# Optimization experiments

Measured on AMD Instinct MI355X. Metric: run time of the kernel, lower is better.

Reference implementation:

```python
import jax, jax.numpy as jnp
import numpy as np

B = 32768
T = 1024  # num_time_bins


def setup_inputs() -> dict:
    key = jax.random.key(0)
    k1, k2, k3, k4 = jax.random.split(key, 4)
    hazard_values = jax.random.uniform(k1, (B, T), dtype=jnp.float32)
    labels_Y = jax.random.uniform(k2, (B,), dtype=jnp.float32) * T
    # nn.Linear(T, T): weight [T, T] (out, in), bias [T]
    lim = 1.0 / np.sqrt(T)
    W = jax.random.uniform(k3, (T, T), minval=-lim, maxval=lim, dtype=jnp.float32)
    b = jax.random.uniform(k4, (T,), minval=-lim, maxval=lim, dtype=jnp.float32)
    return {"hazard_values": hazard_values, "labels_Y": labels_Y, "W": W, "b": b}


def reference(hazard_values, labels_Y, W, b):
    # linear + sigmoid + argmax -> per-row truncation position
    logits = hazard_values @ W.T + b                       # [B, T]
    trunc_pos = jnp.argmax(jax.nn.sigmoid(logits), axis=1, keepdims=True)  # [B, 1] int
    # survival curve
    S = jnp.cumprod(1.0 - hazard_values, axis=1)           # [B, T]
    # vectorized truncation decay: for t >= p, multiply by exp(-(t - p))
    t = jnp.arange(T)[None, :]                             # [1, T]
    decay = jnp.where(t >= trunc_pos,
                      jnp.exp(-(t - trunc_pos).astype(S.dtype)),
                      jnp.ones((), S.dtype))
    S = S * decay
    # MSE between argmax position and labels (original prints; we skip prints)
    p = trunc_pos[:, 0].astype(jnp.float32)
    truncation_loss = jnp.mean((p - labels_Y) ** 2)
    return trunc_pos, S, truncation_loss
```

## Files before the change

kernel.cpp:

```cpp
#include <hip/hip_runtime.h>

#define B_ROWS 32768
#define T_BINS 1024

typedef __attribute__((ext_vector_type(8))) _Float16 half8;
typedef __attribute__((ext_vector_type(4))) float floatx4;

__device__ __forceinline__ unsigned long long pack_max(float v, int col) {
    unsigned x = __float_as_uint(v);
    x = (x & 0x80000000u) ? ~x : (x | 0x80000000u);
    return ((unsigned long long)x << 32) | (unsigned)(~col);
}

__device__ __forceinline__ void async16h(const _Float16* g, _Float16* l) {
    __builtin_amdgcn_global_load_lds(
        (const __attribute__((address_space(1))) unsigned int*)g,
        (__attribute__((address_space(3))) unsigned int*)l,
        16, 0, 0);
}

__global__ __launch_bounds__(256) void tof16_kernel(
    const float* __restrict__ src, _Float16* __restrict__ dst, int n4)
{
    int idx = blockIdx.x * 256 + threadIdx.x;
    if (idx >= n4) return;
    float4 x = ((const float4*)src)[idx];
    union { _Float16 h[4]; ushort4 u; } cv;
    cv.h[0] = (_Float16)x.x;
    cv.h[1] = (_Float16)x.y;
    cv.h[2] = (_Float16)x.z;
    cv.h[3] = (_Float16)x.w;
    ((ushort4*)dst)[idx] = cv.u;
}

__global__ __launch_bounds__(512, 2) void gemm_argmax_f16(
    const float* __restrict__ A, const _Float16* __restrict__ Wh,
    const float* __restrict__ bias, unsigned long long* __restrict__ rec)
{
    __shared__ _Float16 sA[2][256 * 64];
    __shared__ _Float16 sW[2][256 * 64];

    const int tid  = threadIdx.x;
    const int lane = tid & 63;
    const int w    = tid >> 6;
    const int wr   = w >> 1;
    const int wcl  = w & 1;
    const int slab = blockIdx.x >> 2;
    const int cq   = blockIdx.x & 3;

    const int arow = tid >> 1;
    const int part = tid & 1;
    const int x8a  = (arow ^ (arow >> 3)) & 7;
    const float* Abase = A + (size_t)(slab * 256 + arow) * T_BINS;

    const int l3  = lane >> 3;
    const int wsl = lane & 7;

    const int l15 = lane & 15;
    const int hi  = lane >> 4;

    floatx4 acc[4][8];
#pragma unroll
    for (int i = 0; i < 4; ++i)
#pragma unroll
        for (int j = 0; j < 8; ++j) acc[i][j] = (floatx4){0.f, 0.f, 0.f, 0.f};

#pragma unroll
    for (int s = 0; s < 4; ++s) {
        int ps = part * 4 + s;
        int sc = ps ^ x8a;
        float4 f0 = *(const float4*)(Abase + sc * 8);
        float4 f1 = *(const float4*)(Abase + sc * 8 + 4);
        half8 hv;
        hv[0] = (_Float16)f0.x; hv[1] = (_Float16)f0.y; hv[2] = (_Float16)f0.z; hv[3] = (_Float16)f0.w;
        hv[4] = (_Float16)f1.x; hv[5] = (_Float16)f1.y; hv[6] = (_Float16)f1.z; hv[7] = (_Float16)f1.w;
        *(half8*)&sA[0][arow * 64 + ps * 8] = hv;
    }
#pragma unroll
    for (int r = 0; r < 4; ++r) {
        int cl = w * 32 + r * 8 + l3;
        int sk = wsl ^ ((cl ^ (cl >> 3)) & 7);
        async16h(Wh + (size_t)(cq * 256 + cl) * T_BINS + sk * 8,
                 &sW[0][(w * 32 + r * 8) * 64]);
    }
    __syncthreads();

    for (int t = 0; t < 16; ++t) {
        const int cur = t & 1;
        const int nxt = cur ^ 1;
        const int kn  = ((t + 1) & 15) * 64;

        float4 qa0[4], qa1[4];
#pragma unroll
        for (int s = 0; s < 4; ++s) {
            int sc = (part * 4 + s) ^ x8a;
            qa0[s] = *(const float4*)(Abase + kn + sc * 8);
            qa1[s] = *(const float4*)(Abase + kn + sc * 8 + 4);
        }

#pragma unroll
        for (int r = 0; r < 4; ++r) {
            int cl = w * 32 + r * 8 + l3;
            int sk = wsl ^ ((cl ^ (cl >> 3)) & 7);
            async16h(Wh + (size_t)(cq * 256 + cl) * T_BINS + kn + sk * 8,
                     &sW[nxt][(w * 32 + r * 8) * 64]);
        }

#pragma unroll
        for (int g = 0; g < 2; ++g) {
            half8 ah[4];
#pragma unroll
            for (int i = 0; i < 4; ++i) {
                int rl = wr * 64 + i * 16 + l15;
                int xa = (rl ^ (rl >> 3)) & 7;
                ah[i] = *(const half8*)&sA[cur][rl * 64 + (((g * 4 + hi) ^ xa) * 8)];
            }
#pragma unroll
            for (int jb = 0; jb < 2; ++jb) {
                half8 whf[4];
#pragma unroll
                for (int jj = 0; jj < 4; ++jj) {
                    int cl = wcl * 128 + (jb * 4 + jj) * 16 + l15;
                    int xw = (cl ^ (cl >> 3)) & 7;
                    whf[jj] = *(const half8*)&sW[cur][cl * 64 + (((g * 4 + hi) ^ xw) * 8)];
                }
#pragma unroll
                for (int i = 0; i < 4; ++i)
#pragma unroll
                    for (int jj = 0; jj < 4; ++jj)
                        acc[i][jb * 4 + jj] = __builtin_amdgcn_mfma_f32_16x16x32_f16(
                            ah[i], whf[jj], acc[i][jb * 4 + jj], 0, 0, 0);
            }
        }

#pragma unroll
        for (int s = 0; s < 4; ++s) {
            half8 hv;
            hv[0] = (_Float16)qa0[s].x; hv[1] = (_Float16)qa0[s].y;
            hv[2] = (_Float16)qa0[s].z; hv[3] = (_Float16)qa0[s].w;
            hv[4] = (_Float16)qa1[s].x; hv[5] = (_Float16)qa1[s].y;
            hv[6] = (_Float16)qa1[s].z; hv[7] = (_Float16)qa1[s].w;
            *(half8*)&sA[nxt][arow * 64 + (part * 4 + s) * 8] = hv;
        }

        __syncthreads();
    }

    const int colbase = cq * 256 + wcl * 128 + l15;
    float bj[8];
#pragma unroll
    for (int j = 0; j < 8; ++j) bj[j] = bias[colbase + j * 16];

    unsigned long long (*cand)[256] = reinterpret_cast<unsigned long long (*)[256]>(&sA[0][0]);

#pragma unroll
    for (int i = 0; i < 4; ++i)
#pragma unroll
        for (int r = 0; r < 4; ++r) {
            float best = -3.4e38f;
            int   bc   = 0;
#pragma unroll
            for (int j = 0; j < 8; ++j) {
                float v = acc[i][j][r] + bj[j];
                if (v > best) { best = v; bc = colbase + j * 16; }
            }
#pragma unroll
            for (int off = 8; off >= 1; off >>= 1) {
                float ov = __shfl_xor(best, off, 64);
                int   oc = __shfl_xor(bc, off, 64);
                if (ov > best || (ov == best && oc < bc)) { best = ov; bc = oc; }
            }
            if (l15 == 0)
                cand[wcl][wr * 64 + i * 16 + hi * 4 + r] = pack_max(best, bc);
        }
    __syncthreads();

    if (tid < 256) {
        unsigned long long m0 = cand[0][tid], m1 = cand[1][tid];
        atomicMax(&rec[slab * 256 + tid], m0 > m1 ? m0 : m1);
    }
}

__global__ __launch_bounds__(256) void finscan_kernel(
    const float* __restrict__ A, const unsigned long long* __restrict__ rec,
    const float* __restrict__ labels, float* __restrict__ out_trunc,
    float* __restrict__ out_S, float* __restrict__ loss_acc)
{
    __shared__ float trunc_s[64];
    const int tid  = threadIdx.x;
    const int lane = tid & 63;
    const int wc   = tid >> 6;
    const int by   = blockIdx.x;

    if (tid < 64) {
        int rowG = by * 64 + tid;
        unsigned col = ~(unsigned)(rec[rowG] & 0xFFFFFFFFull);
        float p = (float)col;
        out_trunc[rowG] = p;
        trunc_s[tid] = p;
        float d = p - labels[rowG];
        float term = d * d * (1.0f / (float)B_ROWS);
#pragma unroll
        for (int off = 32; off >= 1; off >>= 1)
            term += __shfl_down(term, off, 64);
        if (tid == 0) atomicAdd(loss_acc, term);
    }
    __syncthreads();

    for (int rr = 0; rr < 16; ++rr) {
        int row  = wc * 16 + rr;
        int rowG = by * 64 + row;
        const float* Hrow = A + (size_t)rowG * T_BINS + lane * 16;
        float4 h0 = *(const float4*)(Hrow + 0);
        float4 h1 = *(const float4*)(Hrow + 4);
        float4 h2 = *(const float4*)(Hrow + 8);
        float4 h3 = *(const float4*)(Hrow + 12);
        float hv[16] = {h0.x, h0.y, h0.z, h0.w, h1.x, h1.y, h1.z, h1.w,
                        h2.x, h2.y, h2.z, h2.w, h3.x, h3.y, h3.z, h3.w};
        float vprod[16];
        float run = 1.f;
#pragma unroll
        for (int j = 0; j < 16; ++j) { run *= (1.f - hv[j]); vprod[j] = run; }
        float x = run;
#pragma unroll
        for (int off = 1; off < 64; off <<= 1) {
            float o = __shfl_up(x, off, 64);
            if (lane >= off) x *= o;
        }
        float pre = __shfl_up(x, 1, 64);
        if (lane == 0) pre = 1.f;

        int p  = (int)trunc_s[row];
        int t0 = lane * 16;
        float sv[16];
#pragma unroll
        for (int j = 0; j < 16; ++j) {
            float s = pre * vprod[j];
            int t = t0 + j;
            if (t >= p) s *= __expf((float)(p - t));
            sv[j] = s;
        }
        float* Srow = out_S + (size_t)rowG * T_BINS + lane * 16;
        *(float4*)(Srow + 0)  = (float4){sv[0],  sv[1],  sv[2],  sv[3]};
        *(float4*)(Srow + 4)  = (float4){sv[4],  sv[5],  sv[6],  sv[7]};
        *(float4*)(Srow + 8)  = (float4){sv[8],  sv[9],  sv[10], sv[11]};
        *(float4*)(Srow + 12) = (float4){sv[12], sv[13], sv[14], sv[15]};
    }
}

__global__ __launch_bounds__(256, 2) void mega_kernel(
    const float* __restrict__ A, const _Float16* __restrict__ Wh,
    const float* __restrict__ bias, const float* __restrict__ labels,
    float* __restrict__ out_trunc, float* __restrict__ out_S,
    float* __restrict__ loss_acc)
{
    __shared__ _Float16 sA[2][64 * 64];
    __shared__ _Float16 sW[2][256 * 64];

    const int tid  = threadIdx.x;
    const int lane = tid & 63;
    const int wc   = tid >> 6;
    const int by   = blockIdx.x;

    const int arow = tid >> 2;
    const int ac   = tid & 3;
    const int x8a  = (arow ^ (arow >> 3)) & 7;
    const int sAw0 = arow * 64 + (((ac * 2) ^ x8a) * 8);
    const int sAw1 = arow * 64 + (((ac * 2 + 1) ^ x8a) * 8);
    const float* Abase = A + (size_t)(by * 64 + arow) * T_BINS + ac * 16;

    const int l3   = lane >> 3;
    const int wsl  = lane & 7;

    const int l15  = lane & 15;
    const int hi   = lane >> 4;
    const int xc   = (l15 & 7) ^ (l15 >> 3);

    float run_best[4][4];
    int   run_col[4][4];
#pragma unroll
    for (int i = 0; i < 4; ++i)
#pragma unroll
        for (int r = 0; r < 4; ++r) { run_best[i][r] = -3.4e38f; run_col[i][r] = 0; }

    {
        float4 f0 = *(const float4*)(Abase + 0);
        float4 f1 = *(const float4*)(Abase + 4);
        float4 f2 = *(const float4*)(Abase + 8);
        float4 f3 = *(const float4*)(Abase + 12);
        half8 h0, h1;
        h0[0] = (_Float16)f0.x; h0[1] = (_Float16)f0.y; h0[2] = (_Float16)f0.z; h0[3] = (_Float16)f0.w;
        h0[4] = (_Float16)f1.x; h0[5] = (_Float16)f1.y; h0[6] = (_Float16)f1.z; h0[7] = (_Float16)f1.w;
        h1[0] = (_Float16)f2.x; h1[1] = (_Float16)f2.y; h1[2] = (_Float16)f2.z; h1[3] = (_Float16)f2.w;
        h1[4] = (_Float16)f3.x; h1[5] = (_Float16)f3.y; h1[6] = (_Float16)f3.z; h1[7] = (_Float16)f3.w;
        *(half8*)&sA[0][sAw0] = h0;
        *(half8*)&sA[0][sAw1] = h1;
    }
#pragma unroll
    for (int r = 0; r < 8; ++r)
        async16h(Wh + (size_t)(wc * 64 + r * 8 + l3) * T_BINS + ((wsl ^ l3 ^ r) * 8),
                 &sW[0][(wc * 64 + r * 8) * 64]);
    float4 pa0 = *(const float4*)(Abase + 64);
    float4 pa1 = *(const float4*)(Abase + 68);
    float4 pa2 = *(const float4*)(Abase + 72);
    float4 pa3 = *(const float4*)(Abase + 76);
    __syncthreads();

    int n = 0;
    for (int bx = 0; bx < 4; ++bx) {
        const int colbase = bx * 256 + wc * 64 + l15;
        float bj[4];
#pragma unroll
        for (int j = 0; j < 4; ++j) bj[j] = bias[colbase + j * 16];

        floatx4 acc[4][4];
#pragma unroll
        for (int i = 0; i < 4; ++i)
#pragma unroll
            for (int j = 0; j < 4; ++j) acc[i][j] = (floatx4){0.f, 0.f, 0.f, 0.f};

        for (int t = 0; t < 16; ++t, ++n) {
            const int cur = n & 1;
            const int nxt = cur ^ 1;
            const int m   = (n + 1) & 63;
            const int bxn = m >> 4;
            const int k0n = (m & 15) * 64;

            const int kq = ((n + 2) & 15) * 64;
            float4 qa0 = *(const float4*)(Abase + kq + 0);
            float4 qa1 = *(const float4*)(Abase + kq + 4);
            float4 qa2 = *(const float4*)(Abase + kq + 8);
            float4 qa3 = *(const float4*)(Abase + kq + 12);

#pragma unroll
            for (int r = 0; r < 8; ++r)
                async16h(Wh + (size_t)(bxn * 256 + wc * 64 + r * 8 + l3) * T_BINS
                            + k0n + ((wsl ^ l3 ^ r) * 8),
                         &sW[nxt][(wc * 64 + r * 8) * 64]);

            {
                half8 h0, h1;
                h0[0] = (_Float16)pa0.x; h0[1] = (_Float16)pa0.y; h0[2] = (_Float16)pa0.z; h0[3] = (_Float16)pa0.w;
                h0[4] = (_Float16)pa1.x; h0[5] = (_Float16)pa1.y; h0[6] = (_Float16)pa1.z; h0[7] = (_Float16)pa1.w;
                h1[0] = (_Float16)pa2.x; h1[1] = (_Float16)pa2.y; h1[2] = (_Float16)pa2.z; h1[3] = (_Float16)pa2.w;
                h1[4] = (_Float16)pa3.x; h1[5] = (_Float16)pa3.y; h1[6] = (_Float16)pa3.z; h1[7] = (_Float16)pa3.w;
                *(half8*)&sA[nxt][sAw0] = h0;
                *(half8*)&sA[nxt][sAw1] = h1;
            }
            pa0 = qa0; pa1 = qa1; pa2 = qa2; pa3 = qa3;

#pragma unroll
            for (int g = 0; g < 2; ++g) {
                half8 ah[4], whf[4];
#pragma unroll
                for (int i = 0; i < 4; ++i)
                    ah[i] = *(const half8*)&sA[cur][(i * 16 + l15) * 64
                                                    + (((g * 4 + hi) ^ xc ^ (i * 2)) * 8)];
#pragma unroll
                for (int j = 0; j < 4; ++j)
                    whf[j] = *(const half8*)&sW[cur][(wc * 64 + j * 16 + l15) * 64
                                                     + (((g * 4 + hi) ^ xc ^ (j * 2)) * 8)];
#pragma unroll
                for (int i = 0; i < 4; ++i)
#pragma unroll
                    for (int j = 0; j < 4; ++j)
                        acc[i][j] = __builtin_amdgcn_mfma_f32_16x16x32_f16(ah[i], whf[j], acc[i][j], 0, 0, 0);
            }

            __syncthreads();
        }

#pragma unroll
        for (int i = 0; i < 4; ++i)
#pragma unroll
            for (int r = 0; r < 4; ++r)
#pragma unroll
                for (int j = 0; j < 4; ++j) {
                    float v = acc[i][j][r] + bj[j];
                    if (v > run_best[i][r]) { run_best[i][r] = v; run_col[i][r] = colbase + j * 16; }
                }
    }

    unsigned long long (*cand)[64] = reinterpret_cast<unsigned long long (*)[64]>(&sA[0][0]);
    float* trunc_s = reinterpret_cast<float*>(&sA[0][0]) + 512;

#pragma unroll
    for (int i = 0; i < 4; ++i)
#pragma unroll
        for (int r = 0; r < 4; ++r) {
            float best = run_best[i][r];
            int   bc   = run_col[i][r];
#pragma unroll
            for (int off = 8; off >= 1; off >>= 1) {
                float ov = __shfl_xor(best, off, 64);
                int   oc = __shfl_xor(bc, off, 64);
                if (ov > best || (ov == best && oc < bc)) { best = ov; bc = oc; }
            }
            if ((lane & 15) == 0)
                cand[wc][i * 16 + (lane >> 4) * 4 + r] = pack_max(best, bc);
        }
    __syncthreads();

    if (tid < 64) {
        unsigned long long m01 = cand[0][tid] > cand[1][tid] ? cand[0][tid] : cand[1][tid];
        unsigned long long m23 = cand[2][tid] > cand[3][tid] ? cand[2][tid] : cand[3][tid];
        unsigned long long mm = m01 > m23 ? m01 : m23;
        unsigned col = ~(unsigned)mm;
        float p = (float)col;
        int rowG = by * 64 + tid;
        out_trunc[rowG] = p;
        trunc_s[tid] = p;
        float d = p - labels[rowG];
        float term = d * d * (1.0f / (float)B_ROWS);
#pragma unroll
        for (int off = 32; off >= 1; off >>= 1)
            term += __shfl_down(term, off, 64);
        if (tid == 0) atomicAdd(loss_acc, term);
    }
    __syncthreads();

    for (int rr = 0; rr < 16; ++rr) {
        int row  = wc * 16 + rr;
        int rowG = by * 64 + row;
        const float* Hrow = A + (size_t)rowG * T_BINS + lane * 16;
        float4 h0 = *(const float4*)(Hrow + 0);
        float4 h1 = *(const float4*)(Hrow + 4);
        float4 h2 = *(const float4*)(Hrow + 8);
        float4 h3 = *(const float4*)(Hrow + 12);
        float hv[16] = {h0.x, h0.y, h0.z, h0.w, h1.x, h1.y, h1.z, h1.w,
                        h2.x, h2.y, h2.z, h2.w, h3.x, h3.y, h3.z, h3.w};
        float vprod[16];
        float run = 1.f;
#pragma unroll
        for (int j = 0; j < 16; ++j) { run *= (1.f - hv[j]); vprod[j] = run; }
        float x = run;
#pragma unroll
        for (int off = 1; off < 64; off <<= 1) {
            float o = __shfl_up(x, off, 64);
            if (lane >= off) x *= o;
        }
        float pre = __shfl_up(x, 1, 64);
        if (lane == 0) pre = 1.f;

        int p  = (int)trunc_s[row];
        int t0 = lane * 16;
        float sv[16];
#pragma unroll
        for (int j = 0; j < 16; ++j) {
            float s = pre * vprod[j];
            int t = t0 + j;
            if (t >= p) s *= __expf((float)(p - t));
            sv[j] = s;
        }
        float* Srow = out_S + (size_t)rowG * T_BINS + lane * 16;
        *(float4*)(Srow + 0)  = (float4){sv[0],  sv[1],  sv[2],  sv[3]};
        *(float4*)(Srow + 4)  = (float4){sv[4],  sv[5],  sv[6],  sv[7]};
        *(float4*)(Srow + 8)  = (float4){sv[8],  sv[9],  sv[10], sv[11]};
        *(float4*)(Srow + 12) = (float4){sv[12], sv[13], sv[14], sv[15]};
    }
}

#define BMf 64
#define BKf 16
#define LDSS (BMf + 4)
__global__ __launch_bounds__(256) void gemm_argmax_fp32(
    const float* __restrict__ A, const float* __restrict__ W,
    const float* __restrict__ bias, unsigned long long* __restrict__ rec)
{
    __shared__ float As[BKf][LDSS];
    __shared__ float Ws[BKf][LDSS];
    const int tid = threadIdx.x;
    const int tx = tid & 15, ty = tid >> 4;
    const int bx = blockIdx.x, by = blockIdx.y;
    const int ar = tid >> 2, ak = (tid & 3) << 2;
    const float* Arow = A + (size_t)(by * BMf + ar) * T_BINS + ak;
    const float* Wrow = W + (size_t)(bx * BMf + ar) * T_BINS + ak;
    float acc[4][4];
#pragma unroll
    for (int i = 0; i < 4; ++i)
#pragma unroll
        for (int j = 0; j < 4; ++j) acc[i][j] = 0.f;
    for (int k0 = 0; k0 < T_BINS; k0 += BKf) {
        float4 av = *(const float4*)(Arow + k0);
        float4 wvv = *(const float4*)(Wrow + k0);
        As[ak + 0][ar] = av.x; As[ak + 1][ar] = av.y; As[ak + 2][ar] = av.z; As[ak + 3][ar] = av.w;
        Ws[ak + 0][ar] = wvv.x; Ws[ak + 1][ar] = wvv.y; Ws[ak + 2][ar] = wvv.z; Ws[ak + 3][ar] = wvv.w;
        __syncthreads();
#pragma unroll
        for (int k = 0; k < BKf; ++k) {
            float4 a4 = *(const float4*)&As[k][ty * 4];
            float4 w4 = *(const float4*)&Ws[k][tx * 4];
            float aa[4] = {a4.x, a4.y, a4.z, a4.w};
            float ww[4] = {w4.x, w4.y, w4.z, w4.w};
#pragma unroll
            for (int i = 0; i < 4; ++i)
#pragma unroll
                for (int j = 0; j < 4; ++j) acc[i][j] = fmaf(aa[i], ww[j], acc[i][j]);
        }
        __syncthreads();
    }
    const int colBase = bx * BMf + tx * 4;
    float bv[4];
#pragma unroll
    for (int j = 0; j < 4; ++j) bv[j] = bias[colBase + j];
#pragma unroll
    for (int i = 0; i < 4; ++i) {
        float best = acc[i][0] + bv[0];
        int bc = colBase;
#pragma unroll
        for (int j = 1; j < 4; ++j) {
            float v = acc[i][j] + bv[j];
            if (v > best) { best = v; bc = colBase + j; }
        }
#pragma unroll
        for (int off = 8; off >= 1; off >>= 1) {
            float ov = __shfl_xor(best, off, 64);
            int oc = __shfl_xor(bc, off, 64);
            if (ov > best || (ov == best && oc < bc)) { best = ov; bc = oc; }
        }
        if (tx == 0) atomicMax(&rec[by * BMf + ty * 4 + i], pack_max(best, bc));
    }
}

__global__ __launch_bounds__(256) void finalize_kernel(
    const unsigned long long* __restrict__ rec, const float* __restrict__ labels,
    float* __restrict__ out_trunc, float* __restrict__ loss_acc)
{
    int i = blockIdx.x * 256 + threadIdx.x;
    unsigned col = ~(unsigned)(rec[i] & 0xFFFFFFFFull);
    float p = (float)col;
    out_trunc[i] = p;
    float d = p - labels[i];
    float term = d * d * (1.0f / (float)B_ROWS);
#pragma unroll
    for (int off = 32; off >= 1; off >>= 1)
        term += __shfl_down(term, off, 64);
    __shared__ float partials[4];
    int lane = threadIdx.x & 63, wv = threadIdx.x >> 6;
    if (lane == 0) partials[wv] = term;
    __syncthreads();
    if (threadIdx.x == 0)
        atomicAdd(loss_acc, partials[0] + partials[1] + partials[2] + partials[3]);
}

__global__ __launch_bounds__(256) void scan_kernel_f32(
    const float* __restrict__ H, const float* __restrict__ trunc_f,
    float* __restrict__ Sout)
{
    const int row = blockIdx.x;
    const int tid = threadIdx.x;
    const int lane = tid & 63;
    const int wv = tid >> 6;
    const float4 h = *(const float4*)(H + (size_t)row * T_BINS + tid * 4);
    float l0 = 1.f - h.x;
    float l1 = l0 * (1.f - h.y);
    float l2 = l1 * (1.f - h.z);
    float l3 = l2 * (1.f - h.w);
    float x = l3;
#pragma unroll
    for (int off = 1; off < 64; off <<= 1) {
        float o = __shfl_up(x, off, 64);
        if (lane >= off) x *= o;
    }
    float ex = __shfl_up(x, 1, 64);
    if (lane == 0) ex = 1.f;
    __shared__ float wtot[4];
    if (lane == 63) wtot[wv] = x;
    __syncthreads();
    float wpre = 1.f;
#pragma unroll
    for (int w = 0; w < 3; ++w)
        if (w < wv) wpre *= wtot[w];
    float pre = wpre * ex;
    int p = (int)trunc_f[row];
    int t0 = tid * 4;
    float sv[4] = {pre * l0, pre * l1, pre * l2, pre * l3};
#pragma unroll
    for (int j = 0; j < 4; ++j) {
        int t = t0 + j;
        if (t >= p) sv[j] *= __expf((float)(p - t));
    }
    float4 s4 = {sv[0], sv[1], sv[2], sv[3]};
    *(float4*)(Sout + (size_t)row * T_BINS + tid * 4) = s4;
}

extern "C" void kernel_launch(void* const* d_in, const int* in_sizes, int n_in,
                              void* d_out, int out_size, void* d_ws, size_t ws_size,
                              hipStream_t stream)
{
    const float* hazard = (const float*)d_in[0];
    const float* labels = (const float*)d_in[1];
    const float* W      = (const float*)d_in[2];
    const float* bias   = (const float*)d_in[3];

    float* out       = (float*)d_out;
    float* out_trunc = out;
    float* out_S     = out + B_ROWS;
    float* out_loss  = out + B_ROWS + (size_t)B_ROWS * T_BINS;

    hipMemsetAsync(out_loss, 0, sizeof(float), stream);

    const size_t NW = (size_t)T_BINS * T_BINS;
    const size_t wh_bytes  = NW * sizeof(_Float16);
    const size_t rec_bytes = (size_t)B_ROWS * sizeof(unsigned long long);

    if (ws_size >= wh_bytes + rec_bytes) {
        _Float16* Wh = (_Float16*)d_ws;
        unsigned long long* rec = (unsigned long long*)((char*)d_ws + wh_bytes);
        hipMemsetAsync(rec, 0, rec_bytes, stream);
        tof16_kernel<<<(int)(NW / 4 / 256), 256, 0, stream>>>(W, Wh, (int)(NW / 4));
        gemm_argmax_f16<<<512, 512, 0, stream>>>(hazard, Wh, bias, rec);
        finscan_kernel<<<512, 256, 0, stream>>>(hazard, rec, labels, out_trunc, out_S, out_loss);
    } else if (ws_size >= wh_bytes) {
        _Float16* Wh = (_Float16*)d_ws;
        tof16_kernel<<<(int)(NW / 4 / 256), 256, 0, stream>>>(W, Wh, (int)(NW / 4));
        mega_kernel<<<B_ROWS / 64, 256, 0, stream>>>(
            hazard, Wh, bias, labels, out_trunc, out_S, out_loss);
    } else {
        unsigned long long* rec = (unsigned long long*)out_S;
        hipMemsetAsync(rec, 0, (size_t)B_ROWS * sizeof(unsigned long long), stream);
        dim3 ggrid(T_BINS / BMf, B_ROWS / BMf);
        gemm_argmax_fp32<<<ggrid, 256, 0, stream>>>(hazard, W, bias, rec);
        finalize_kernel<<<B_ROWS / 256, 256, 0, stream>>>(rec, labels, out_trunc, out_loss);
        scan_kernel_f32<<<B_ROWS, 256, 0, stream>>>(hazard, out_trunc, out_S);
    }
}
```

Before: 387.5 us.

## Restructure f16 GEMM-argmax into 128-row blocks sweeping 512 columns with running max

```diff
diff --git a/kernel.cpp b/kernel.cpp
--- a/kernel.cpp
+++ b/kernel.cpp
@@ -33,25 +33,23 @@
     ((ushort4*)dst)[idx] = cv.u;
 }
 
-__global__ __launch_bounds__(512, 2) void gemm_argmax_f16(
+__global__ __launch_bounds__(256, 2) void gemm_argmax_f16(
     const float* __restrict__ A, const _Float16* __restrict__ Wh,
     const float* __restrict__ bias, unsigned long long* __restrict__ rec)
 {
-    __shared__ _Float16 sA[2][256 * 64];
-    __shared__ _Float16 sW[2][256 * 64];
+    __shared__ _Float16 sA[2][128 * 64];
+    __shared__ _Float16 sW[2][128 * 64];
 
     const int tid  = threadIdx.x;
     const int lane = tid & 63;
     const int w    = tid >> 6;
-    const int wr   = w >> 1;
-    const int wcl  = w & 1;
-    const int slab = blockIdx.x >> 2;
-    const int cq   = blockIdx.x & 3;
+    const int slab = blockIdx.x >> 1;
+    const int ch   = blockIdx.x & 1;
 
     const int arow = tid >> 1;
     const int part = tid & 1;
     const int x8a  = (arow ^ (arow >> 3)) & 7;
-    const float* Abase = A + (size_t)(slab * 256 + arow) * T_BINS;
+    const float* Abase = A + (size_t)(slab * 128 + arow) * T_BINS;
 
     const int l3  = lane >> 3;
     const int wsl = lane & 7;
@@ -59,11 +57,12 @@
     const int l15 = lane & 15;
     const int hi  = lane >> 4;
 
-    floatx4 acc[4][8];
-#pragma unroll
-    for (int i = 0; i < 4; ++i)
-#pragma unroll
-        for (int j = 0; j < 8; ++j) acc[i][j] = (floatx4){0.f, 0.f, 0.f, 0.f};
+    float run_best[8][4];
+    int   run_col[8][4];
+#pragma unroll
+    for (int i = 0; i < 8; ++i)
+#pragma unroll
+        for (int r = 0; r < 4; ++r) { run_best[i][r] = -3.4e38f; run_col[i][r] = 0; }
 
 #pragma unroll
     for (int s = 0; s < 4; ++s) {
@@ -80,90 +79,102 @@
     for (int r = 0; r < 4; ++r) {
         int cl = w * 32 + r * 8 + l3;
         int sk = wsl ^ ((cl ^ (cl >> 3)) & 7);
-        async16h(Wh + (size_t)(cq * 256 + cl) * T_BINS + sk * 8,
+        async16h(Wh + (size_t)(ch * 512 + cl) * T_BINS + sk * 8,
                  &sW[0][(w * 32 + r * 8) * 64]);
     }
     __syncthreads();
 
-    for (int t = 0; t < 16; ++t) {
-        const int cur = t & 1;
-        const int nxt = cur ^ 1;
-        const int kn  = ((t + 1) & 15) * 64;
-
-        float4 qa0[4], qa1[4];
-#pragma unroll
-        for (int s = 0; s < 4; ++s) {
-            int sc = (part * 4 + s) ^ x8a;
-            qa0[s] = *(const float4*)(Abase + kn + sc * 8);
-            qa1[s] = *(const float4*)(Abase + kn + sc * 8 + 4);
-        }
-
+    for (int bxs = 0; bxs < 4; ++bxs) {
+        const int colstage = ch * 512 + bxs * 128 + w * 32 + l15;
+        float bj[2];
+        bj[0] = bias[colstage];
+        bj[1] = bias[colstage + 16];
+
+        floatx4 acc[8][2];
+#pragma unroll
+        for (int i = 0; i < 8; ++i)
+#pragma unroll
+            for (int j = 0; j < 2; ++j) acc[i][j] = (floatx4){0.f, 0.f, 0.f, 0.f};
+
+        for (int t = 0; t < 16; ++t) {
+            const int n    = bxs * 16 + t;
+            const int cur  = n & 1;
+            const int nxt  = cur ^ 1;
+            const int n1   = (n + 1) & 63;
+            const int bxsn = n1 >> 4;
+            const int kn   = (n1 & 15) * 64;
+
+            float4 qa0[4], qa1[4];
+#pragma unroll
+            for (int s = 0; s < 4; ++s) {
+                int sc = (part * 4 + s) ^ x8a;
+                qa0[s] = *(const float4*)(Abase + kn + sc * 8);
+                qa1[s] = *(const float4*)(Abase + kn + sc * 8 + 4);
+            }
+
+#pragma unroll
+            for (int r = 0; r < 4; ++r) {
+                int cl = w * 32 + r * 8 + l3;
+                int sk = wsl ^ ((cl ^ (cl >> 3)) & 7);
+                async16h(Wh + (size_t)(ch * 512 + bxsn * 128 + cl) * T_BINS + kn + sk * 8,
+                         &sW[nxt][(w * 32 + r * 8) * 64]);
+            }
+
+#pragma unroll
+            for (int g = 0; g < 2; ++g) {
+                half8 ah[8], whf[2];
+#pragma unroll
+                for (int i = 0; i < 8; ++i) {
+                    int rl = i * 16 + l15;
+                    int xa = (rl ^ (rl >> 3)) & 7;
+                    ah[i] = *(const half8*)&sA[cur][rl * 64 + (((g * 4 + hi) ^ xa) * 8)];
+                }
+#pragma unroll
+                for (int j = 0; j < 2; ++j) {
+                    int cl = w * 32 + j * 16 + l15;
+                    int xw = (cl ^ (cl >> 3)) & 7;
+                    whf[j] = *(const half8*)&sW[cur][cl * 64 + (((g * 4 + hi) ^ xw) * 8)];
+                }
+#pragma unroll
+                for (int i = 0; i < 8; ++i)
+#pragma unroll
+                    for (int j = 0; j < 2; ++j)
+                        acc[i][j] = __builtin_amdgcn_mfma_f32_16x16x32_f16(
+                            ah[i], whf[j], acc[i][j], 0, 0, 0);
+            }
+
+#pragma unroll
+            for (int s = 0; s < 4; ++s) {
+                half8 hv;
+                hv[0] = (_Float16)qa0[s].x; hv[1] = (_Float16)qa0[s].y;
+                hv[2] = (_Float16)qa0[s].z; hv[3] = (_Float16)qa0[s].w;
+                hv[4] = (_Float16)qa1[s].x; hv[5] = (_Float16)qa1[s].y;
+                hv[6] = (_Float16)qa1[s].z; hv[7] = (_Float16)qa1[s].w;
+                *(half8*)&sA[nxt][arow * 64 + (part * 4 + s) * 8] = hv;
+            }
+
+            __syncthreads();
+        }
+
+#pragma unroll
+        for (int i = 0; i < 8; ++i)
+#pragma unroll
+            for (int r = 0; r < 4; ++r)
+#pragma unroll
+                for (int j = 0; j < 2; ++j) {
+                    float v = acc[i][j][r] + bj[j];
+                    if (v > run_best[i][r]) { run_best[i][r] = v; run_col[i][r] = colstage + j * 16; }
+                }
+    }
+
+    unsigned long long (*cand)[128] = reinterpret_cast<unsigned long long (*)[128]>(&sA[0][0]);
+
+#pragma unroll
+    for (int i = 0; i < 8; ++i)
 #pragma unroll
         for (int r = 0; r < 4; ++r) {
-            int cl = w * 32 + r * 8 + l3;
-            int sk = wsl ^ ((cl ^ (cl >> 3)) & 7);
-            async16h(Wh + (size_t)(cq * 256 + cl) * T_BINS + kn + sk * 8,
-                     &sW[nxt][(w * 32 + r * 8) * 64]);
-        }
-
-#pragma unroll
-        for (int g = 0; g < 2; ++g) {
-            half8 ah[4];
-#pragma unroll
-            for (int i = 0; i < 4; ++i) {
-                int rl = wr * 64 + i * 16 + l15;
-                int xa = (rl ^ (rl >> 3)) & 7;
-                ah[i] = *(const half8*)&sA[cur][rl * 64 + (((g * 4 + hi) ^ xa) * 8)];
-            }
-#pragma unroll
-            for (int jb = 0; jb < 2; ++jb) {
-                half8 whf[4];
-#pragma unroll
-                for (int jj = 0; jj < 4; ++jj) {
-                    int cl = wcl * 128 + (jb * 4 + jj) * 16 + l15;
-                    int xw = (cl ^ (cl >> 3)) & 7;
-                    whf[jj] = *(const half8*)&sW[cur][cl * 64 + (((g * 4 + hi) ^ xw) * 8)];
-                }
-#pragma unroll
-                for (int i = 0; i < 4; ++i)
-#pragma unroll
-                    for (int jj = 0; jj < 4; ++jj)
-                        acc[i][jb * 4 + jj] = __builtin_amdgcn_mfma_f32_16x16x32_f16(
-                            ah[i], whf[jj], acc[i][jb * 4 + jj], 0, 0, 0);
-            }
-        }
-
-#pragma unroll
-        for (int s = 0; s < 4; ++s) {
-            half8 hv;
-            hv[0] = (_Float16)qa0[s].x; hv[1] = (_Float16)qa0[s].y;
-            hv[2] = (_Float16)qa0[s].z; hv[3] = (_Float16)qa0[s].w;
-            hv[4] = (_Float16)qa1[s].x; hv[5] = (_Float16)qa1[s].y;
-            hv[6] = (_Float16)qa1[s].z; hv[7] = (_Float16)qa1[s].w;
-            *(half8*)&sA[nxt][arow * 64 + (part * 4 + s) * 8] = hv;
-        }
-
-        __syncthreads();
-    }
-
-    const int colbase = cq * 256 + wcl * 128 + l15;
-    float bj[8];
-#pragma unroll
-    for (int j = 0; j < 8; ++j) bj[j] = bias[colbase + j * 16];
-
-    unsigned long long (*cand)[256] = reinterpret_cast<unsigned long long (*)[256]>(&sA[0][0]);
-
-#pragma unroll
-    for (int i = 0; i < 4; ++i)
-#pragma unroll
-        for (int r = 0; r < 4; ++r) {
-            float best = -3.4e38f;
-            int   bc   = 0;
-#pragma unroll
-            for (int j = 0; j < 8; ++j) {
-                float v = acc[i][j][r] + bj[j];
-                if (v > best) { best = v; bc = colbase + j * 16; }
-            }
+            float best = run_best[i][r];
+            int   bc   = run_col[i][r];
 #pragma unroll
             for (int off = 8; off >= 1; off >>= 1) {
                 float ov = __shfl_xor(best, off, 64);
@@ -171,13 +182,15 @@
                 if (ov > best || (ov == best && oc < bc)) { best = ov; bc = oc; }
             }
             if (l15 == 0)
-                cand[wcl][wr * 64 + i * 16 + hi * 4 + r] = pack_max(best, bc);
-        }
-    __syncthreads();
-
-    if (tid < 256) {
-        unsigned long long m0 = cand[0][tid], m1 = cand[1][tid];
-        atomicMax(&rec[slab * 256 + tid], m0 > m1 ? m0 : m1);
+                cand[w][i * 16 + hi * 4 + r] = pack_max(best, bc);
+        }
+    __syncthreads();
+
+    if (tid < 128) {
+        unsigned long long m01 = cand[0][tid] > cand[1][tid] ? cand[0][tid] : cand[1][tid];
+        unsigned long long m23 = cand[2][tid] > cand[3][tid] ? cand[2][tid] : cand[3][tid];
+        unsigned long long mm  = m01 > m23 ? m01 : m23;
+        atomicMax(&rec[slab * 128 + tid], mm);
     }
 }
 
@@ -609,7 +622,7 @@
         unsigned long long* rec = (unsigned long long*)((char*)d_ws + wh_bytes);
         hipMemsetAsync(rec, 0, rec_bytes, stream);
         tof16_kernel<<<(int)(NW / 4 / 256), 256, 0, stream>>>(W, Wh, (int)(NW / 4));
-        gemm_argmax_f16<<<512, 512, 0, stream>>>(hazard, Wh, bias, rec);
+        gemm_argmax_f16<<<512, 256, 0, stream>>>(hazard, Wh, bias, rec);
         finscan_kernel<<<512, 256, 0, stream>>>(hazard, rec, labels, out_trunc, out_S, out_loss);
     } else if (ws_size >= wh_bytes) {
         _Float16* Wh = (_Float16*)d_ws;
```

Measured after the change: 461.3 us. 19.1% more time.
